# Optimization experiments

Hardware: AMD Instinct MI355X
Metric: run time of the kernel (lower is better)

Reference implementation:

```python
import jax, jax.numpy as jnp
import numpy as np

DIM = 96; NH = 3; HD = DIM // NH; SCALE = HD ** -0.5
WS = (7, 7, 7); N = WS[0] * WS[1] * WS[2]
SHIFT = (3, 3, 3)  # half window
NL = 2
GRID = (28, 28, 28)
B = 2


def _rel_index():
    wd, wh, ww = WS
    coords = np.stack(np.meshgrid(np.arange(wd), np.arange(wh), np.arange(ww), indexing='ij')).reshape(3, -1)
    rel = (coords[:, :, None] - coords[:, None, :]).transpose(1, 2, 0)  # [N,N,3]
    rel[..., 0] += wd - 1; rel[..., 1] += wh - 1; rel[..., 2] += ww - 1
    rel[..., 0] *= (2 * wh - 1) * (2 * ww - 1); rel[..., 1] *= (2 * ww - 1)
    return rel.sum(-1)  # [N,N]

REL_IDX = _rel_index()


def _window_partition(x):
    b, D, H, W, C = x.shape
    wd, wh, ww = WS
    x = x.reshape(b, D // wd, wd, H // wh, wh, W // ww, ww, C)
    x = x.transpose(0, 1, 3, 5, 2, 4, 6, 7)
    return x.reshape(-1, N, C)


def _window_reverse(win, b, D, H, W):
    wd, wh, ww = WS
    C = win.shape[-1]
    x = win.reshape(b, D // wd, H // wh, W // ww, wd, wh, ww, C)
    x = x.transpose(0, 1, 4, 2, 5, 3, 6, 7)
    return x.reshape(b, D, H, W, C)


def _compute_mask():
    # MONAI compute_mask for the shifted (SW-MSA) block
    D, H, W = GRID; wd, wh, ww = WS; sd, sh, sw = SHIFT
    img = np.zeros((1, D, H, W, 1), np.float32)
    cnt = 0
    for d in (slice(-wd), slice(-wd, -sd), slice(-sd, None)):
        for h in (slice(-wh), slice(-wh, -sh), slice(-sh, None)):
            for w in (slice(-ww), slice(-ww, -sw), slice(-sw, None)):
                img[:, d, h, w, :] = cnt; cnt += 1
    mw = img.reshape(1, D // wd, wd, H // wh, wh, W // ww, ww, 1)
    mw = mw.transpose(0, 1, 3, 5, 2, 4, 6, 7).reshape(-1, N)  # [nw, N]
    am = mw[:, None, :] - mw[:, :, None]
    return np.where(am != 0, np.float32(-100.0), np.float32(0.0))

MASK = jnp.asarray(_compute_mask())  # [nw, N, N]


def _ln(x, g, b):
    mu = x.mean(-1, keepdims=True)
    var = ((x - mu) ** 2).mean(-1, keepdims=True)
    return (x - mu) / jnp.sqrt(var + 1e-5) * g + b


def _block(x, p, shift, mask):
    b, D, H, W, C = x.shape
    h = _ln(x, p['n1g'], p['n1b'])
    if shift is not None:
        h = jnp.roll(h, (-shift[0], -shift[1], -shift[2]), axis=(1, 2, 3))
    xw = _window_partition(h)  # [b*nw, N, C]
    Bn = xw.shape[0]
    qkv = (xw @ p['qkvw'].T + p['qkvb']).reshape(Bn, N, 3, NH, HD).transpose(2, 0, 3, 1, 4)
    q, k, v = qkv[0] * SCALE, qkv[1], qkv[2]
    attn = jnp.einsum('bhnd,bhmd->bhnm', q, k)
    bias = p['rel'][REL_IDX.reshape(-1)].reshape(N, N, NH).transpose(2, 0, 1)
    attn = attn + bias[None]
    if mask is not None:
        nw = mask.shape[0]
        attn = (attn.reshape(Bn // nw, nw, NH, N, N) + mask[None, :, None]).reshape(Bn, NH, N, N)
    attn = jax.nn.softmax(attn, axis=-1)
    out = jnp.einsum('bhnm,bhmd->bhnd', attn, v).transpose(0, 2, 1, 3).reshape(Bn, N, C)
    out = out @ p['projw'].T + p['projb']
    h = _window_reverse(out, b, D, H, W)
    if shift is not None:
        h = jnp.roll(h, shift, axis=(1, 2, 3))
    x = x + h
    m = _ln(x, p['n2g'], p['n2b'])
    m = jax.nn.gelu(m @ p['fc1w'].T + p['fc1b'], approximate=False) @ p['fc2w'].T + p['fc2b']
    return x + m


def setup_inputs() -> dict:
    key = jax.random.key(0)
    ks = jax.random.split(key, 8)
    nbias = (2 * WS[0] - 1) * (2 * WS[1] - 1) * (2 * WS[2] - 1)
    return {
        'x': jax.random.normal(ks[0], (B,) + GRID + (DIM,), jnp.float32),
        'norm1_g': jnp.ones((NL, DIM), jnp.float32),
        'norm1_b': jnp.zeros((NL, DIM), jnp.float32),
        'qkv_w': jax.random.normal(ks[1], (NL, 3 * DIM, DIM), jnp.float32) * 0.02,
        'qkv_b': jnp.zeros((NL, 3 * DIM), jnp.float32),
        'rel_bias': jax.random.normal(ks[2], (NL, nbias, NH), jnp.float32) * 0.02,
        'proj_w': jax.random.normal(ks[3], (NL, DIM, DIM), jnp.float32) * 0.02,
        'proj_b': jnp.zeros((NL, DIM), jnp.float32),
        'norm2_g': jnp.ones((NL, DIM), jnp.float32),
        'norm2_b': jnp.zeros((NL, DIM), jnp.float32),
        'fc1_w': jax.random.normal(ks[4], (NL, 4 * DIM, DIM), jnp.float32) * 0.02,
        'fc1_b': jnp.zeros((NL, 4 * DIM), jnp.float32),
        'fc2_w': jax.random.normal(ks[5], (NL, DIM, 4 * DIM), jnp.float32) * 0.02,
        'fc2_b': jnp.zeros((NL, DIM), jnp.float32),
    }


def reference(x, norm1_g, norm1_b, qkv_w, qkv_b, rel_bias, proj_w, proj_b,
              norm2_g, norm2_b, fc1_w, fc1_b, fc2_w, fc2_b):
    for i in range(NL):
        p = dict(n1g=norm1_g[i], n1b=norm1_b[i], qkvw=qkv_w[i], qkvb=qkv_b[i],
                 rel=rel_bias[i], projw=proj_w[i], projb=proj_b[i],
                 n2g=norm2_g[i], n2b=norm2_b[i], fc1w=fc1_w[i], fc1b=fc1_b[i],
                 fc2w=fc2_w[i], fc2b=fc2_b[i])
        if i % 2 == 0:
            x = _block(x, p, None, None)  # W-MSA (mask is all-zero for shift=0)
        else:
            x = _block(x, p, SHIFT, MASK)  # SW-MSA
    return x
```

## Files before the change

kernel.cpp:

```cpp
#include <hip/hip_runtime.h>
#include <math.h>

#define DIM 96
#define NHD 3
#define HD 32
#define NWT 343
#define NWIN 128
#define TOK 43904
#define NBIAS 2197
#define SCALE 0.17677669529663687f
#define TPAD 352

typedef __attribute__((ext_vector_type(8))) short bf16x8;
typedef __attribute__((ext_vector_type(4))) float f32x4;

__device__ __forceinline__ unsigned short f2b(float f) {
    union { float f; unsigned int u; } x; x.f = f;
    unsigned int r = (x.u + 0x7fffu + ((x.u >> 16) & 1u)) >> 16;
    return (unsigned short)r;
}
__device__ __forceinline__ unsigned int pk2bf(float a, float b) {
    union { float f; unsigned int u; } x, y; x.f = a; y.f = b;
    return ((x.u + 0x8000u) >> 16) | ((y.u + 0x8000u) & 0xffff0000u);
}

__global__ void __launch_bounds__(256) k_cvt4(
        const float* __restrict__ s0, const float* __restrict__ s1,
        const float* __restrict__ s2, const float* __restrict__ s3,
        unsigned short* __restrict__ dst) {
    int i = blockIdx.x * 256 + threadIdx.x;
    if (i >= 221184) return;
    const float* src; int off;
    if (i < 55296)       { src = s0; off = i; }
    else if (i < 73728)  { src = s1; off = i - 55296; }
    else if (i < 147456) { src = s2; off = i - 73728; }
    else                 { src = s3; off = i - 147456; }
    dst[i] = f2b(src[off]);
}

__global__ void __launch_bounds__(256) k_qkv(
        const float* __restrict__ x, const float* __restrict__ g1,
        const float* __restrict__ b1, const unsigned short* __restrict__ W,
        const float* __restrict__ bias, unsigned short* __restrict__ q,
        unsigned short* __restrict__ k, unsigned short* __restrict__ v, int shift) {
    __shared__ __align__(16) unsigned short lns[64][104];
    __shared__ __align__(16) unsigned short wbuf[96][104];
    int wid = threadIdx.x >> 6, lane = threadIdx.x & 63;
    int lm = lane & 15, q4 = lane >> 4;
    int m0 = blockIdx.x * 64 + wid * 16;
    int bwr[4], nnr[4];
    size_t rowoff[4];
    #pragma unroll
    for (int r = 0; r < 4; ++r) {
        int wtok = m0 + q4 * 4 + r;
        int bw = wtok / NWT, n = wtok % NWT;
        bwr[r] = bw; nnr[r] = n;
        int b = bw >> 6, win = bw & 63;
        int wdi = win >> 4, whi = (win >> 2) & 3, wwi = win & 3;
        int d = n / 49, h = (n / 7) % 7, w = n % 7;
        int sd = (wdi * 7 + d + shift) % 28;
        int sh = (whi * 7 + h + shift) % 28;
        int sw = (wwi * 7 + w + shift) % 28;
        rowoff[r] = (((size_t)(b * 28 + sd) * 28 + sh) * 28 + sw) * 96;
    }
    float val[6][4], g1v[6], b1v[6];
    #pragma unroll
    for (int c = 0; c < 6; ++c) {
        int ncol = c * 16 + lm;
        g1v[c] = g1[ncol]; b1v[c] = b1[ncol];
        #pragma unroll
        for (int r = 0; r < 4; ++r) val[c][r] = x[rowoff[r] + ncol];
    }
    #pragma unroll
    for (int r = 0; r < 4; ++r) {
        float s = 0.f, s2 = 0.f;
        #pragma unroll
        for (int c = 0; c < 6; ++c) { s += val[c][r]; s2 += val[c][r] * val[c][r]; }
        #pragma unroll
        for (int off = 8; off > 0; off >>= 1) {
            s  += __shfl_xor(s,  off, 64);
            s2 += __shfl_xor(s2, off, 64);
        }
        float mu = s * (1.0f / 96.0f);
        float rstd = rsqrtf(s2 * (1.0f / 96.0f) - mu * mu + 1e-5f);
        int row = wid * 16 + q4 * 4 + r;
        #pragma unroll
        for (int c = 0; c < 6; ++c)
            lns[row][c * 16 + lm] = f2b((val[c][r] - mu) * rstd * g1v[c] + b1v[c]);
    }
    __syncthreads();
    bf16x8 a1[3];
    #pragma unroll
    for (int ks = 0; ks < 3; ++ks)
        a1[ks] = *((const bf16x8*)&lns[wid * 16 + lm][ks * 32 + q4 * 8]);
    for (int ch = 0; ch < 3; ++ch) {
        __syncthreads();
        const uint4* src = (const uint4*)(W + ch * 96 * 96);
        for (int s = threadIdx.x; s < 1152; s += 256) {
            int row = s / 12, seg = s % 12;
            *((uint4*)&wbuf[row][seg * 8]) = src[s];
        }
        __syncthreads();
        f32x4 acc[6];
        #pragma unroll
        for (int c = 0; c < 6; ++c) acc[c] = (f32x4){0.f, 0.f, 0.f, 0.f};
        #pragma unroll
        for (int ks = 0; ks < 3; ++ks) {
            #pragma unroll
            for (int c = 0; c < 6; ++c) {
                bf16x8 b = *((const bf16x8*)&wbuf[c * 16 + lm][ks * 32 + q4 * 8]);
                acc[c] = __builtin_amdgcn_mfma_f32_16x16x32_bf16(a1[ks], b, acc[c], 0, 0, 0);
            }
        }
        #pragma unroll
        for (int c = 0; c < 6; ++c) {
            int col = c * 16 + lm;
            int head = col >> 5, hd = col & 31;
            float bb = bias[ch * 96 + col];
            #pragma unroll
            for (int r = 0; r < 4; ++r) {
                int wh = bwr[r] * NHD + head;
                float vv = acc[c][r] + bb;
                if (ch == 0)
                    q[(size_t)wh * (TPAD * 32) + nnr[r] * 32 + hd] = f2b(vv * SCALE);
                else if (ch == 1)
                    k[(size_t)wh * (TPAD * 32) + nnr[r] * 32 + hd] = f2b(vv);
                else
                    v[(size_t)wh * (32 * TPAD) + hd * TPAD + nnr[r]] = f2b(vv);
            }
        }
    }
}

__global__ void __launch_bounds__(256) k_attn(
        const unsigned short* __restrict__ q, const unsigned short* __restrict__ k,
        const unsigned short* __restrict__ vT, const float* __restrict__ rel,
        unsigned short* __restrict__ o, int shifted) {
    __shared__ float relh[NBIAS];
    __shared__ int   jinfo[NWT];
    __shared__ __align__(16) unsigned short vts[32 * 360];
    __shared__ __align__(16) unsigned short pbuf[4][2][16 * 40];
    __shared__ float dnm[4][2][16];
    int wh = blockIdx.x / 3, third = blockIdx.x % 3;
    int bw = wh / NHD, head = wh % NHD;
    for (int i = threadIdx.x; i < NBIAS; i += 256) relh[i] = rel[i * NHD + head];
    const unsigned int* vsrc = (const unsigned int*)(vT + (size_t)wh * 32 * TPAD);
    unsigned int* vdst = (unsigned int*)vts;
    for (int i = threadIdx.x; i < 32 * 176; i += 256) {
        int row = i / 176, cc = i - row * 176;
        vdst[row * 180 + cc] = vsrc[i];
    }
    int win = bw & 63;
    int wdi = win >> 4, whi = (win >> 2) & 3, wwi = win & 3;
    for (int i = threadIdx.x; i < NWT; i += 256) {
        int d = i / 49, h = (i / 7) % 7, w = i % 7;
        int gd = wdi * 7 + d, gh = whi * 7 + h, gw = wwi * 7 + w;
        int rd = (gd < 21) ? 0 : ((gd < 25) ? 1 : 2);
        int rh = (gh < 21) ? 0 : ((gh < 25) ? 1 : 2);
        int rw = (gw < 21) ? 0 : ((gw < 25) ? 1 : 2);
        jinfo[i] = (d * 169 + h * 13 + w) | ((rd * 9 + rh * 3 + rw) << 16);
    }
    __syncthreads();
    int wid = threadIdx.x >> 6, lane = threadIdx.x & 63;
    int lm = lane & 15, q4 = lane >> 4;
    int tb = third * 8 + wid * 2;
    if (tb > 21) return;
    bool dual = (tb + 1 <= 21);
    int qtA = tb, qtB = dual ? tb + 1 : tb;
    const unsigned short* qbase = q + (size_t)wh * TPAD * 32;
    const unsigned short* kbase = k + (size_t)wh * TPAD * 32;
    int qtokA = qtA * 16 + lm, qtokB = qtB * 16 + lm;
    bf16x8 qfA = *((const bf16x8*)(qbase + qtokA * 32 + q4 * 8));
    bf16x8 qfB = *((const bf16x8*)(qbase + qtokB * 32 + q4 * 8));
    int jqA = jinfo[min(qtokA, NWT - 1)], jqB = jinfo[min(qtokB, NWT - 1)];
    int jqcA = (jqA & 0xffff) + 1098, rqA = jqA >> 16;
    int jqcB = (jqB & 0xffff) + 1098, rqB = jqB >> 16;
    f32x4 aA0 = (f32x4){0.f,0.f,0.f,0.f}, aA1 = aA0, aB0 = aA0, aB1 = aA0;
    float dA = 0.f, dB = 0.f;
    unsigned short* pbA = pbuf[wid][0];
    unsigned short* pbB = pbuf[wid][1];
    for (int pr = 0; pr < 11; ++pr) {
        int kb0 = pr * 32;
        bf16x8 kf0 = *((const bf16x8*)(kbase + (kb0 + lm) * 32 + q4 * 8));
        bf16x8 kf1 = *((const bf16x8*)(kbase + (kb0 + 16 + lm) * 32 + q4 * 8));
        f32x4 z = (f32x4){0.f, 0.f, 0.f, 0.f};
        f32x4 sA0 = __builtin_amdgcn_mfma_f32_16x16x32_bf16(kf0, qfA, z, 0, 0, 0);
        f32x4 sA1 = __builtin_amdgcn_mfma_f32_16x16x32_bf16(kf1, qfA, z, 0, 0, 0);
        f32x4 sB0 = __builtin_amdgcn_mfma_f32_16x16x32_bf16(kf0, qfB, z, 0, 0, 0);
        f32x4 sB1 = __builtin_amdgcn_mfma_f32_16x16x32_bf16(kf1, qfB, z, 0, 0, 0);
        float pA[8], pB[8];
        #pragma unroll
        for (int t = 0; t < 2; ++t) {
            #pragma unroll
            for (int r = 0; r < 4; ++r) {
                int key = kb0 + t * 16 + q4 * 4 + r;
                int jk = jinfo[min(key, NWT - 1)];
                int jkc = jk & 0xffff, rk = jk >> 16;
                bool pad = key >= NWT;
                float sA_ = (t ? sA1[r] : sA0[r]) + relh[jqcA - jkc];
                if (shifted && (rk != rqA)) sA_ -= 100.0f;
                float pvA = pad ? 0.0f : __expf(sA_);
                dA += pvA; pA[t * 4 + r] = pvA;
                float sB_ = (t ? sB1[r] : sB0[r]) + relh[jqcB - jkc];
                if (shifted && (rk != rqB)) sB_ -= 100.0f;
                float pvB = pad ? 0.0f : __expf(sB_);
                dB += pvB; pB[t * 4 + r] = pvB;
            }
        }
        #pragma unroll
        for (int t = 0; t < 2; ++t) {
            *((unsigned int*)(pbA + lm * 40 + t * 16 + q4 * 4)) =
                pk2bf(pA[t * 4 + 0], pA[t * 4 + 1]);
            *((unsigned int*)(pbA + lm * 40 + t * 16 + q4 * 4 + 2)) =
                pk2bf(pA[t * 4 + 2], pA[t * 4 + 3]);
            *((unsigned int*)(pbB + lm * 40 + t * 16 + q4 * 4)) =
                pk2bf(pB[t * 4 + 0], pB[t * 4 + 1]);
            *((unsigned int*)(pbB + lm * 40 + t * 16 + q4 * 4 + 2)) =
                pk2bf(pB[t * 4 + 2], pB[t * 4 + 3]);
        }
        bf16x8 pfA = *((const bf16x8*)(pbA + lm * 40 + q4 * 8));
        bf16x8 pfB = *((const bf16x8*)(pbB + lm * 40 + q4 * 8));
        bf16x8 v0 = *((const bf16x8*)(vts + lm * 360 + kb0 + q4 * 8));
        bf16x8 v1 = *((const bf16x8*)(vts + (16 + lm) * 360 + kb0 + q4 * 8));
        aA0 = __builtin_amdgcn_mfma_f32_16x16x32_bf16(pfA, v0, aA0, 0, 0, 0);
        aA1 = __builtin_amdgcn_mfma_f32_16x16x32_bf16(pfA, v1, aA1, 0, 0, 0);
        aB0 = __builtin_amdgcn_mfma_f32_16x16x32_bf16(pfB, v0, aB0, 0, 0, 0);
        aB1 = __builtin_amdgcn_mfma_f32_16x16x32_bf16(pfB, v1, aB1, 0, 0, 0);
    }
    dA += __shfl_xor(dA, 16, 64); dA += __shfl_xor(dA, 32, 64);
    dB += __shfl_xor(dB, 16, 64); dB += __shfl_xor(dB, 32, 64);
    if (lane < 16) { dnm[wid][0][lm] = dA; dnm[wid][1][lm] = dB; }
    #pragma unroll
    for (int r = 0; r < 4; ++r) {
        int qrowA = qtA * 16 + q4 * 4 + r;
        if (qrowA < NWT) {
            float inv = 1.0f / dnm[wid][0][q4 * 4 + r];
            unsigned short* op = o + (size_t)(bw * NWT + qrowA) * DIM + head * HD;
            op[lm]      = f2b(aA0[r] * inv);
            op[16 + lm] = f2b(aA1[r] * inv);
        }
    }
    if (dual) {
        #pragma unroll
        for (int r = 0; r < 4; ++r) {
            int qrowB = qtB * 16 + q4 * 4 + r;
            if (qrowB < NWT) {
                float inv = 1.0f / dnm[wid][1][q4 * 4 + r];
                unsigned short* op = o + (size_t)(bw * NWT + qrowB) * DIM + head * HD;
                op[lm]      = f2b(aB0[r] * inv);
                op[16 + lm] = f2b(aB1[r] * inv);
            }
        }
    }
}

__global__ void __launch_bounds__(256) k_pm(
        const unsigned short* __restrict__ ao, const unsigned short* __restrict__ Wp,
        const float* __restrict__ pbias, const float* __restrict__ xin,
        float* __restrict__ xout,
        const float* __restrict__ g2, const float* __restrict__ b2,
        const unsigned short* __restrict__ w1, const float* __restrict__ bb1,
        const unsigned short* __restrict__ w2, const float* __restrict__ bb2,
        int shift) {
    __shared__ __align__(16) unsigned short lns[64][104];
    __shared__ __align__(16) unsigned short big[18816];
    int wid = threadIdx.x >> 6, lane = threadIdx.x & 63;
    int lm = lane & 15, q4 = lane >> 4;
    int m0 = blockIdx.x * 64 + wid * 16;
    for (int s = threadIdx.x; s < 1152; s += 256) {
        int row = s / 12, seg = s % 12;
        *((uint4*)&big[row * 104 + seg * 8]) = ((const uint4*)Wp)[s];
    }
    const unsigned short* arow = ao + (size_t)(m0 + lm) * 96;
    bf16x8 a1[3];
    #pragma unroll
    for (int ks = 0; ks < 3; ++ks)
        a1[ks] = *((const bf16x8*)(arow + ks * 32 + q4 * 8));
    __syncthreads();
    f32x4 acc[6];
    #pragma unroll
    for (int c = 0; c < 6; ++c) acc[c] = (f32x4){0.f, 0.f, 0.f, 0.f};
    #pragma unroll
    for (int ks = 0; ks < 3; ++ks) {
        #pragma unroll
        for (int c = 0; c < 6; ++c) {
            bf16x8 b = *((const bf16x8*)&big[(c * 16 + lm) * 104 + ks * 32 + q4 * 8]);
            acc[c] = __builtin_amdgcn_mfma_f32_16x16x32_bf16(a1[ks], b, acc[c], 0, 0, 0);
        }
    }
    size_t rowoff[4];
    #pragma unroll
    for (int r = 0; r < 4; ++r) {
        int wtok = m0 + q4 * 4 + r;
        int bw = wtok / NWT, n = wtok % NWT;
        int b = bw >> 6, win = bw & 63;
        int wdi = win >> 4, whi = (win >> 2) & 3, wwi = win & 3;
        int d = n / 49, h = (n / 7) % 7, w = n % 7;
        int sd = (wdi * 7 + d + shift) % 28;
        int sh = (whi * 7 + h + shift) % 28;
        int sw = (wwi * 7 + w + shift) % 28;
        rowoff[r] = (((size_t)(b * 28 + sd) * 28 + sh) * 28 + sw) * 96;
    }
    float val[6][4], g2v[6], b2v[6];
    #pragma unroll
    for (int c = 0; c < 6; ++c) {
        int n = c * 16 + lm;
        float bb = pbias[n];
        g2v[c] = g2[n]; b2v[c] = b2[n];
        #pragma unroll
        for (int r = 0; r < 4; ++r)
            val[c][r] = xin[rowoff[r] + n] + acc[c][r] + bb;
    }
    #pragma unroll
    for (int r = 0; r < 4; ++r) {
        float s = 0.f, s2 = 0.f;
        #pragma unroll
        for (int c = 0; c < 6; ++c) { s += val[c][r]; s2 += val[c][r] * val[c][r]; }
        #pragma unroll
        for (int off = 8; off > 0; off >>= 1) {
            s  += __shfl_xor(s,  off, 64);
            s2 += __shfl_xor(s2, off, 64);
        }
        float mu = s * (1.0f / 96.0f);
        float rstd = rsqrtf(s2 * (1.0f / 96.0f) - mu * mu + 1e-5f);
        int row = wid * 16 + q4 * 4 + r;
        #pragma unroll
        for (int c = 0; c < 6; ++c)
            lns[row][c * 16 + lm] = f2b((val[c][r] - mu) * rstd * g2v[c] + b2v[c]);
    }
    bf16x8 am[3];
    #pragma unroll
    for (int ks = 0; ks < 3; ++ks)
        am[ks] = *((const bf16x8*)&lns[wid * 16 + lm][ks * 32 + q4 * 8]);
    f32x4 acc2[6];
    #pragma unroll
    for (int c = 0; c < 6; ++c) acc2[c] = (f32x4){0.f, 0.f, 0.f, 0.f};
    unsigned short* hid_ = &big[13952 + wid * 1216];
    for (int ch = 0; ch < 6; ++ch) {
        __syncthreads();
        const uint4* src1 = (const uint4*)(w1 + ch * 64 * 96);
        #pragma unroll
        for (int t = 0; t < 3; ++t) {
            int s = threadIdx.x + t * 256;
            int row = s / 12, seg = s % 12;
            *((uint4*)&big[row * 104 + seg * 8]) = src1[s];
        }
        #pragma unroll
        for (int t = 0; t < 3; ++t) {
            int s = threadIdx.x + t * 256;
            int row = s >> 3, seg = s & 7;
            *((uint4*)&big[6656 + row * 76 + seg * 8]) =
                *((const uint4*)(w2 + row * 384 + ch * 64 + seg * 8));
        }
        __syncthreads();
        f32x4 acc1[4];
        #pragma unroll
        for (int t = 0; t < 4; ++t) acc1[t] = (f32x4){0.f, 0.f, 0.f, 0.f};
        #pragma unroll
        for (int ks = 0; ks < 3; ++ks) {
            #pragma unroll
            for (int t = 0; t < 4; ++t) {
                bf16x8 b = *((const bf16x8*)&big[(t * 16 + lm) * 104 + ks * 32 + q4 * 8]);
                acc1[t] = __builtin_amdgcn_mfma_f32_16x16x32_bf16(am[ks], b, acc1[t], 0, 0, 0);
            }
        }
        #pragma unroll
        for (int t = 0; t < 4; ++t) {
            float bb = bb1[ch * 64 + t * 16 + lm];
            #pragma unroll
            for (int r = 0; r < 4; ++r) {
                float v2 = acc1[t][r] + bb;
                float ge = 0.5f * v2 * (1.0f + erff(v2 * 0.70710678118654752f));
                hid_[(q4 * 4 + r) * 76 + t * 16 + lm] = f2b(ge);
            }
        }
        #pragma unroll
        for (int ks2 = 0; ks2 < 2; ++ks2) {
            bf16x8 a = *((const bf16x8*)(hid_ + lm * 76 + ks2 * 32 + q4 * 8));
            #pragma unroll
            for (int c = 0; c < 6; ++c) {
                bf16x8 b = *((const bf16x8*)&big[6656 + (c * 16 + lm) * 76 + ks2 * 32 + q4 * 8]);
                acc2[c] = __builtin_amdgcn_mfma_f32_16x16x32_bf16(a, b, acc2[c], 0, 0, 0);
            }
        }
    }
    #pragma unroll
    for (int c = 0; c < 6; ++c) {
        int n = c * 16 + lm;
        float bb = bb2[n];
        #pragma unroll
        for (int r = 0; r < 4; ++r)
            xout[rowoff[r] + n] = val[c][r] + acc2[c][r] + bb;
    }
}

extern "C" void kernel_launch(void* const* d_in, const int* in_sizes, int n_in,
                              void* d_out, int out_size, void* d_ws, size_t ws_size,
                              hipStream_t stream) {
    const float* x     = (const float*)d_in[0];
    const float* n1g   = (const float*)d_in[1];
    const float* n1b   = (const float*)d_in[2];
    const float* qkvw  = (const float*)d_in[3];
    const float* qkvb  = (const float*)d_in[4];
    const float* relb  = (const float*)d_in[5];
    const float* projw = (const float*)d_in[6];
    const float* projb = (const float*)d_in[7];
    const float* n2g   = (const float*)d_in[8];
    const float* n2b   = (const float*)d_in[9];
    const float* fc1w  = (const float*)d_in[10];
    const float* fc1b  = (const float*)d_in[11];
    const float* fc2w  = (const float*)d_in[12];
    const float* fc2b  = (const float*)d_in[13];
    float* out = (float*)d_out;

    const size_t NEL = (size_t)TOK * DIM;
    const size_t QKN = (size_t)NWIN * NHD * TPAD * 32;
    float* buf_x = (float*)d_ws;
    unsigned short* hbuf = (unsigned short*)(buf_x + NEL);
    unsigned short* bq   = hbuf + NEL;
    unsigned short* bk   = bq + QKN;
    unsigned short* bv   = bk + QKN;
    unsigned short* wts  = bv + QKN;
    unsigned short* wq  = wts;
    unsigned short* wp  = wq + 2 * 27648;
    unsigned short* w1  = wp + 2 * 9216;
    unsigned short* w2  = w1 + 2 * 36864;

    k_cvt4<<<(221184 + 255) / 256, 256, 0, stream>>>(qkvw, projw, fc1w, fc2w, wts);

    for (int L = 0; L < 2; ++L) {
        int shift = (L == 0) ? 0 : 3;
        const float* xin_l = (L == 0) ? x : buf_x;
        float* xfin = (L == 0) ? buf_x : out;

        k_qkv<<<TOK / 64, 256, 0, stream>>>(xin_l, n1g + L * 96, n1b + L * 96,
                                            wq + L * 27648, qkvb + L * 288,
                                            bq, bk, bv, shift);
        k_attn<<<NWIN * NHD * 3, 256, 0, stream>>>(bq, bk, bv, relb + L * NBIAS * NHD, hbuf,
                                                   shift ? 1 : 0);
        k_pm<<<TOK / 64, 256, 0, stream>>>(hbuf, wp + L * 9216, projb + L * 96,
                                           xin_l, xfin,
                                           n2g + L * 96, n2b + L * 96,
                                           w1 + L * 36864, fc1b + L * 384,
                                           w2 + L * 36864, fc2b + L * 96, shift);
    }
}
```

Baseline: 269.7 us.

## Precompute dense relative-bias+mask tables per window type in a setup kernel

Adds a setup kernel that expands the relative position bias and the shifted-window mask into dense [type][head][343][352] float tables. Padded key columns are set to a large negative value, so the attention loop no longer needs its per-key jinfo lookup, LDS bias gather, mask compare and pad select. Each attention block now reads bias rows straight from global memory as float4 loads, and its shared-memory bias staging is removed. The cost is about 13 MB of extra table traffic per layer, served from L2 or HBM, instead of LDS lookups, plus one more kernel launch.

After: 291.2 us. 8.0% more time.

```diff
diff --git a/kernel.cpp b/kernel.cpp
--- a/kernel.cpp
+++ b/kernel.cpp
@@ -10,6 +10,7 @@
 #define NBIAS 2197
 #define SCALE 0.17677669529663687f
 #define TPAD 352
+#define TSZ  (343 * 352)
 
 typedef __attribute__((ext_vector_type(8))) short bf16x8;
 typedef __attribute__((ext_vector_type(4))) float f32x4;
@@ -36,6 +37,39 @@
     else if (i < 147456) { src = s2; off = i - 73728; }
     else                 { src = s3; off = i - 147456; }
     dst[i] = f2b(src[off]);
+}
+
+__global__ void __launch_bounds__(256) k_bias(
+        const float* __restrict__ rel0, const float* __restrict__ rel1,
+        float* __restrict__ bt) {
+    int i = blockIdx.x * 256 + threadIdx.x;
+    if (i >= 9 * 3 * 343 * 352) return;
+    int kcol = i % 352;
+    int t = i / 352;
+    int q = t % 343; t /= 343;
+    int head = t % 3; int combo = t / 3;
+    float outv;
+    if (kcol >= 343) {
+        outv = -100000.0f;
+    } else {
+        int dq = q / 49, hq = (q / 7) % 7, wq = q % 7;
+        int dk = kcol / 49, hk = (kcol / 7) % 7, wk = kcol % 7;
+        int ridx = (dq - dk + 6) * 169 + (hq - hk + 6) * 13 + (wq - wk + 6);
+        const float* rel = (combo == 0) ? rel0 : rel1;
+        float b = rel[ridx * 3 + head];
+        if (combo > 0) {
+            int ty = combo - 1;
+            int rqd = (ty & 4) ? 1 + (dq >= 4) : 0;
+            int rqh = (ty & 2) ? 1 + (hq >= 4) : 0;
+            int rqw = (ty & 1) ? 1 + (wq >= 4) : 0;
+            int rkd = (ty & 4) ? 1 + (dk >= 4) : 0;
+            int rkh = (ty & 2) ? 1 + (hk >= 4) : 0;
+            int rkw = (ty & 1) ? 1 + (wk >= 4) : 0;
+            if (rqd != rkd || rqh != rkh || rqw != rkw) b -= 100.0f;
+        }
+        outv = b;
+    }
+    bt[i] = outv;
 }
 
 __global__ void __launch_bounds__(256) k_qkv(
@@ -134,33 +168,24 @@
 
 __global__ void __launch_bounds__(256) k_attn(
         const unsigned short* __restrict__ q, const unsigned short* __restrict__ k,
-        const unsigned short* __restrict__ vT, const float* __restrict__ rel,
-        unsigned short* __restrict__ o, int shifted) {
-    __shared__ float relh[NBIAS];
-    __shared__ int   jinfo[NWT];
+        const unsigned short* __restrict__ vT, const float* __restrict__ bt,
+        unsigned short* __restrict__ o, int tmul) {
     __shared__ __align__(16) unsigned short vts[32 * 360];
     __shared__ __align__(16) unsigned short pbuf[4][2][16 * 40];
     __shared__ float dnm[4][2][16];
     int wh = blockIdx.x / 3, third = blockIdx.x % 3;
     int bw = wh / NHD, head = wh % NHD;
-    for (int i = threadIdx.x; i < NBIAS; i += 256) relh[i] = rel[i * NHD + head];
     const unsigned int* vsrc = (const unsigned int*)(vT + (size_t)wh * 32 * TPAD);
     unsigned int* vdst = (unsigned int*)vts;
     for (int i = threadIdx.x; i < 32 * 176; i += 256) {
         int row = i / 176, cc = i - row * 176;
         vdst[row * 180 + cc] = vsrc[i];
     }
+    __syncthreads();
     int win = bw & 63;
     int wdi = win >> 4, whi = (win >> 2) & 3, wwi = win & 3;
-    for (int i = threadIdx.x; i < NWT; i += 256) {
-        int d = i / 49, h = (i / 7) % 7, w = i % 7;
-        int gd = wdi * 7 + d, gh = whi * 7 + h, gw = wwi * 7 + w;
-        int rd = (gd < 21) ? 0 : ((gd < 25) ? 1 : 2);
-        int rh = (gh < 21) ? 0 : ((gh < 25) ? 1 : 2);
-        int rw = (gw < 21) ? 0 : ((gw < 25) ? 1 : 2);
-        jinfo[i] = (d * 169 + h * 13 + w) | ((rd * 9 + rh * 3 + rw) << 16);
-    }
-    __syncthreads();
+    int type = ((wdi == 3) ? 4 : 0) | ((whi == 3) ? 2 : 0) | ((wwi == 3) ? 1 : 0);
+    const float* bbase = bt + (size_t)type * tmul + (size_t)head * TSZ;
     int wid = threadIdx.x >> 6, lane = threadIdx.x & 63;
     int lm = lane & 15, q4 = lane >> 4;
     int tb = third * 8 + wid * 2;
@@ -172,9 +197,8 @@
     int qtokA = qtA * 16 + lm, qtokB = qtB * 16 + lm;
     bf16x8 qfA = *((const bf16x8*)(qbase + qtokA * 32 + q4 * 8));
     bf16x8 qfB = *((const bf16x8*)(qbase + qtokB * 32 + q4 * 8));
-    int jqA = jinfo[min(qtokA, NWT - 1)], jqB = jinfo[min(qtokB, NWT - 1)];
-    int jqcA = (jqA & 0xffff) + 1098, rqA = jqA >> 16;
-    int jqcB = (jqB & 0xffff) + 1098, rqB = jqB >> 16;
+    const float* bpA = bbase + (size_t)min(qtokA, NWT - 1) * 352;
+    const float* bpB = bbase + (size_t)min(qtokB, NWT - 1) * 352;
     f32x4 aA0 = (f32x4){0.f,0.f,0.f,0.f}, aA1 = aA0, aB0 = aA0, aB1 = aA0;
     float dA = 0.f, dB = 0.f;
     unsigned short* pbA = pbuf[wid][0];
@@ -183,6 +207,10 @@
         int kb0 = pr * 32;
         bf16x8 kf0 = *((const bf16x8*)(kbase + (kb0 + lm) * 32 + q4 * 8));
         bf16x8 kf1 = *((const bf16x8*)(kbase + (kb0 + 16 + lm) * 32 + q4 * 8));
+        f32x4 bA0 = *((const f32x4*)(bpA + kb0 + q4 * 4));
+        f32x4 bA1 = *((const f32x4*)(bpA + kb0 + 16 + q4 * 4));
+        f32x4 bB0 = *((const f32x4*)(bpB + kb0 + q4 * 4));
+        f32x4 bB1 = *((const f32x4*)(bpB + kb0 + 16 + q4 * 4));
         f32x4 z = (f32x4){0.f, 0.f, 0.f, 0.f};
         f32x4 sA0 = __builtin_amdgcn_mfma_f32_16x16x32_bf16(kf0, qfA, z, 0, 0, 0);
         f32x4 sA1 = __builtin_amdgcn_mfma_f32_16x16x32_bf16(kf1, qfA, z, 0, 0, 0);
@@ -190,22 +218,11 @@
         f32x4 sB1 = __builtin_amdgcn_mfma_f32_16x16x32_bf16(kf1, qfB, z, 0, 0, 0);
         float pA[8], pB[8];
         #pragma unroll
-        for (int t = 0; t < 2; ++t) {
-            #pragma unroll
-            for (int r = 0; r < 4; ++r) {
-                int key = kb0 + t * 16 + q4 * 4 + r;
-                int jk = jinfo[min(key, NWT - 1)];
-                int jkc = jk & 0xffff, rk = jk >> 16;
-                bool pad = key >= NWT;
-                float sA_ = (t ? sA1[r] : sA0[r]) + relh[jqcA - jkc];
-                if (shifted && (rk != rqA)) sA_ -= 100.0f;
-                float pvA = pad ? 0.0f : __expf(sA_);
-                dA += pvA; pA[t * 4 + r] = pvA;
-                float sB_ = (t ? sB1[r] : sB0[r]) + relh[jqcB - jkc];
-                if (shifted && (rk != rqB)) sB_ -= 100.0f;
-                float pvB = pad ? 0.0f : __expf(sB_);
-                dB += pvB; pB[t * 4 + r] = pvB;
-            }
+        for (int r = 0; r < 4; ++r) {
+            float a0 = __expf(sA0[r] + bA0[r]); dA += a0; pA[r] = a0;
+            float a1 = __expf(sA1[r] + bA1[r]); dA += a1; pA[4 + r] = a1;
+            float b0 = __expf(sB0[r] + bB0[r]); dB += b0; pB[r] = b0;
+            float b1 = __expf(sB1[r] + bB1[r]); dB += b1; pB[4 + r] = b1;
         }
         #pragma unroll
         for (int t = 0; t < 2; ++t) {
@@ -425,19 +442,23 @@
     unsigned short* wp  = wq + 2 * 27648;
     unsigned short* w1  = wp + 2 * 9216;
     unsigned short* w2  = w1 + 2 * 36864;
+    float* btab = (float*)(wts + 221184);
 
     k_cvt4<<<(221184 + 255) / 256, 256, 0, stream>>>(qkvw, projw, fc1w, fc2w, wts);
+    k_bias<<<(9 * 3 * 343 * 352 + 255) / 256, 256, 0, stream>>>(
+        relb, relb + NBIAS * NHD, btab);
 
     for (int L = 0; L < 2; ++L) {
         int shift = (L == 0) ? 0 : 3;
         const float* xin_l = (L == 0) ? x : buf_x;
         float* xfin = (L == 0) ? buf_x : out;
+        const float* btL = (L == 0) ? btab : btab + 3 * TSZ;
+        int tmul = (L == 0) ? 0 : 3 * TSZ;
 
         k_qkv<<<TOK / 64, 256, 0, stream>>>(xin_l, n1g + L * 96, n1b + L * 96,
                                             wq + L * 27648, qkvb + L * 288,
                                             bq, bk, bv, shift);
-        k_attn<<<NWIN * NHD * 3, 256, 0, stream>>>(bq, bk, bv, relb + L * NBIAS * NHD, hbuf,
-                                                   shift ? 1 : 0);
+        k_attn<<<NWIN * NHD * 3, 256, 0, stream>>>(bq, bk, bv, btL, hbuf, tmul);
         k_pm<<<TOK / 64, 256, 0, stream>>>(hbuf, wp + L * 9216, projb + L * 96,
                                            xin_l, xfin,
                                            n2g + L * 96, n2b + L * 96,
```
